# Performance work log

Hardware: AMD Instinct MI355X
Metric: run time of the kernel (lower is better)

Reference implementation:

```python
import jax, jax.numpy as jnp
import numpy as np

B, S, P, G, E = 16, 1024, 32, 64, 512
HD = E // 2          # head_dim = 256
SCALE = HD ** -0.5
LAMBDA_INIT = 0.8 - 0.6 * float(np.exp(-0.3 * 0.0))  # depth=0 -> 0.2
EPS = 1e-5


def setup_inputs() -> dict:
    key = jax.random.key(0)
    ks = jax.random.split(key, 12)
    inp = {
        'query': jax.random.normal(ks[0], (B, S, E), jnp.float32),
        'key': jax.random.normal(ks[1], (B, P, G, E), jnp.float32),
        'mask': jax.random.randint(ks[2], (B, S), 0, 2).astype(bool),
        'Wq': jax.random.normal(ks[3], (E, E), jnp.float32) * (E ** -0.5),
        'Wk': jax.random.normal(ks[4], (E, E), jnp.float32) * (E ** -0.5),
        'Wv': jax.random.normal(ks[5], (E, E), jnp.float32) * (E ** -0.5),
        'Wo': jax.random.normal(ks[6], (E, E), jnp.float32) * (E ** -0.5),
        'lq1': jax.random.normal(ks[7], (HD,), jnp.float32) * 0.1,
        'lk1': jax.random.normal(ks[8], (HD,), jnp.float32) * 0.1,
        'lq2': jax.random.normal(ks[9], (HD,), jnp.float32) * 0.1,
        'lk2': jax.random.normal(ks[10], (HD,), jnp.float32) * 0.1,
        'gamma': jnp.ones((E,), jnp.float32),
    }
    return inp


def reference(query, key, mask, Wq, Wk, Wv, Wo, lq1, lk1, lq2, lk2, gamma):
    b, s, e = query.shape
    _, p, g, _ = key.shape
    L = p * g
    key2d = key.reshape(b, L, e)

    Q = (query @ Wq).reshape(b, s, 2, HD).transpose(0, 2, 1, 3) * SCALE  # [B,2,S,hd]
    K = (key2d @ Wk).reshape(b, L, 2, HD).transpose(0, 2, 1, 3)          # [B,2,L,hd]
    V = key2d @ Wv                                                       # [B,L,E]

    scores = jnp.einsum('bhsd,bhld->bhsl', Q, K)                         # [B,2,S,L]
    # masked_fill(~mask, 0.0) with mask broadcast [B,1,S,1]
    scores = jnp.where(mask[:, None, :, None], scores, 0.0)
    attn = jax.nn.softmax(scores, axis=-1)

    lam1 = jnp.exp(jnp.sum(lq1 * lk1))
    lam2 = jnp.exp(jnp.sum(lq2 * lk2))
    lam = lam1 - lam2 + LAMBDA_INIT

    diff = attn[:, 0] - lam * attn[:, 1]                                 # [B,S,L]
    out2d = jnp.einsum('bsl,ble->bse', diff, V)                          # [B,S,E]

    # RMSNorm over last dim with affine gamma
    rms = out2d * jax.lax.rsqrt(jnp.mean(out2d * out2d, axis=-1, keepdims=True) + EPS)
    rms = rms * gamma
    out = (rms * (1.0 - LAMBDA_INIT)) @ Wo                               # [B,S,E]

    return out, diff.reshape(b, s, p, g)
```

## Files before the change

kernel.cpp:

```cpp
#include <hip/hip_runtime.h>
#include <hip/hip_bf16.h>


typedef short short8 __attribute__((ext_vector_type(8)));
typedef __bf16 bf16x8 __attribute__((ext_vector_type(8)));
typedef float f32x4 __attribute__((ext_vector_type(4)));

#define LDS_BYTES 16384
#define OUT0_ELEMS 8388608L

__global__ void probe_kernel(const void* gamma, const void* mask, int* flags)
{
    if (threadIdx.x == 0) {
        unsigned g = *(const unsigned*)gamma;
        flags[0] = (g == 0x3F800000u) ? 1 : 0;
        flags[1] = 0;
    }
    __syncthreads();
    const unsigned* mi = (const unsigned*)mask;
    int bad = 0;
    for (int i = threadIdx.x; i < 4096; i += blockDim.x)
        if (mi[i] > 1u) bad = 1;
    if (bad) atomicOr(&flags[1], 1);
}

__global__ void convert_mask(const void* __restrict__ mask, int* __restrict__ mi,
                             const int* __restrict__ flags)
{
    int i = blockIdx.x * 256 + threadIdx.x;
    if (flags[1]) mi[i] = ((const unsigned char*)mask)[i] ? 1 : 0;
    else          mi[i] = ((const int*)mask)[i] ? 1 : 0;
}

__device__ __forceinline__ float read_elem(const void* p, int i, int isf32)
{
    return isf32 ? ((const float*)p)[i]
                 : __bfloat162float(((const __hip_bfloat16*)p)[i]);
}

__global__ void convert_gamma(const void* __restrict__ gamma, float* __restrict__ g,
                              const int* __restrict__ flags)
{
    int i = blockIdx.x * 256 + threadIdx.x;
    g[i] = read_elem(gamma, i, flags[0]);
}

__global__ void transpose_w(const void* __restrict__ Wq, const void* __restrict__ Wk,
                            const void* __restrict__ Wv, const void* __restrict__ Wo,
                            __hip_bfloat16* __restrict__ dst, const int* __restrict__ flags)
{
    int which = blockIdx.y;
    const void* s = (which == 0) ? Wq : (which == 1) ? Wk : (which == 2) ? Wv : Wo;
    __hip_bfloat16* d = dst + (long)which * 262144;
    int idx = blockIdx.x * 256 + threadIdx.x;
    int k = idx >> 9, n = idx & 511;
    d[n * 512 + k] = __float2bfloat16(read_elem(s, idx, flags[0]));
}

__global__ void lam_kernel(const void* __restrict__ lq1, const void* __restrict__ lk1,
                           const void* __restrict__ lq2, const void* __restrict__ lk2,
                           float* __restrict__ lamp, const int* __restrict__ flags)
{
    int t = threadIdx.x;
    int f = flags[0];
    float s1 = 0.0f, s2 = 0.0f;
#pragma unroll
    for (int j = 0; j < 4; ++j) {
        int idx = t * 4 + j;
        s1 += read_elem(lq1, idx, f) * read_elem(lk1, idx, f);
        s2 += read_elem(lq2, idx, f) * read_elem(lk2, idx, f);
    }
#pragma unroll
    for (int off = 1; off < 64; off <<= 1) {
        s1 += __shfl_xor(s1, off);
        s2 += __shfl_xor(s2, off);
    }
    if (t == 0) *lamp = __expf(s1) - __expf(s2) + 0.2f;
}

__global__ void zero_lst(float* __restrict__ lst)
{
    lst[blockIdx.x * 256 + threadIdx.x] = 0.0f;
}

__device__ __forceinline__ void stage_u(const void* A, long aoff, int lda, int af32,
                                        const __hip_bfloat16* B, int ldb,
                                        int kt, char* smem, int tid)
{
    if (af32) {
#pragma unroll
        for (int j = 0; j < 2; ++j) {
            int chunk = j * 256 + tid;
            const float* g = (const float*)A + aoff + (long)(chunk >> 2) * lda + kt + (chunk & 3) * 8;
            f32x4 x0 = *(const f32x4*)g;
            f32x4 x1 = *(const f32x4*)(g + 4);
            __hip_bfloat16 tmp[8];
#pragma unroll
            for (int t = 0; t < 4; ++t) tmp[t] = __float2bfloat16(x0[t]);
#pragma unroll
            for (int t = 0; t < 4; ++t) tmp[4 + t] = __float2bfloat16(x1[t]);
            *(short8*)(smem + chunk * 16) = *(const short8*)tmp;
        }
    } else {
#pragma unroll
        for (int j = 0; j < 2; ++j) {
            int chunk = j * 256 + tid;
            const __hip_bfloat16* g = (const __hip_bfloat16*)A + aoff
                                    + (long)(chunk >> 2) * lda + kt + (chunk & 3) * 8;
            __builtin_amdgcn_global_load_lds(
                (__attribute__((address_space(1))) void*)g,
                (__attribute__((address_space(3))) void*)(smem + chunk * 16), 16, 0, 0);
        }
    }
#pragma unroll
    for (int j = 0; j < 2; ++j) {
        int chunk = j * 256 + tid;
        const __hip_bfloat16* g = B + (long)(chunk >> 2) * ldb + kt + (chunk & 3) * 8;
        __builtin_amdgcn_global_load_lds(
            (__attribute__((address_space(1))) void*)g,
            (__attribute__((address_space(3))) void*)(smem + 8192 + chunk * 16), 16, 0, 0);
    }
}

__device__ __forceinline__ void mfma_block(char* smem, int tid, f32x4 (&acc)[4][4])
{
    const int lane = tid & 63, wid = tid >> 6;
    const int wm = wid >> 1, wn = wid & 1;
    const int lm = lane & 15, lq = lane >> 4;
    short8 a[4], b[4];
#pragma unroll
    for (int i = 0; i < 4; ++i)
        a[i] = *(const short8*)(smem + (wm * 64 + i * 16 + lm) * 64 + lq * 16);
#pragma unroll
    for (int i = 0; i < 4; ++i)
        b[i] = *(const short8*)(smem + 8192 + (wn * 64 + i * 16 + lm) * 64 + lq * 16);
#pragma unroll
    for (int i = 0; i < 4; ++i)
#pragma unroll
        for (int j = 0; j < 4; ++j)
            acc[i][j] = __builtin_amdgcn_mfma_f32_16x16x32_bf16(
                __builtin_bit_cast(bf16x8, a[i]),
                __builtin_bit_cast(bf16x8, b[j]),
                acc[i][j], 0, 0, 0);
}

__device__ __forceinline__ void zero_acc(f32x4 (&acc)[4][4])
{
#pragma unroll
    for (int i = 0; i < 4; ++i)
#pragma unroll
        for (int j = 0; j < 4; ++j)
#pragma unroll
            for (int r = 0; r < 4; ++r) acc[i][j][r] = 0.0f;
}

__device__ __forceinline__ void tile_gemm_u(const void* A, long aoff, int lda, int af32,
                                            const __hip_bfloat16* B, int ldb, int K,
                                            char* smem, int tid, f32x4 (&acc)[4][4])
{
    zero_acc(acc);
    for (int kt = 0; kt < K; kt += 32) {
        __syncthreads();
        stage_u(A, aoff, lda, af32, B, ldb, kt, smem, tid);
        __syncthreads();
        mfma_block(smem, tid, acc);
    }
}

template <int MODE, int AF>
__launch_bounds__(256, 4)
__global__ void gemm_u(const void* __restrict__ A,
                       const __hip_bfloat16* __restrict__ B,
                       void* __restrict__ C,
                       int K, int lda, int ldb, int ldc,
                       long sA, long sB, long sC, float scale,
                       const int* __restrict__ flags)
{
    __shared__ __align__(16) char smem[LDS_BYTES];
    const int tid = threadIdx.x;
    const int bn = blockIdx.x, bm = blockIdx.y, bz = blockIdx.z;
    const int af32 = AF ? flags[0] : 0;
    const long aoff = (long)bz * sA + (long)bm * 128 * lda;
    const __hip_bfloat16* Bb = B + (long)bz * sB + (long)bn * 128 * ldb;

    f32x4 acc[4][4];
    tile_gemm_u(A, aoff, lda, af32, Bb, ldb, K, smem, tid, acc);

    const int f32o = (MODE == 3) ? flags[0] : 0;
    const int lane = tid & 63, wid = tid >> 6;
    const int wm = wid >> 1, wn = wid & 1;
    const int lm = lane & 15, lq = lane >> 4;
#pragma unroll
    for (int im = 0; im < 4; ++im)
#pragma unroll
        for (int in = 0; in < 4; ++in)
#pragma unroll
            for (int r = 0; r < 4; ++r) {
                int row = bm * 128 + wm * 64 + im * 16 + lq * 4 + r;
                int col = bn * 128 + wn * 64 + in * 16 + lm;
                float v = acc[im][in][r] * scale;
                if (MODE == 0) {
                    ((__hip_bfloat16*)C)[bz * sC + (long)row * ldc + col] = __float2bfloat16(v);
                } else if (MODE == 2) {
                    ((float*)C)[bz * sC + (long)row * ldc + col] = v;
                } else if (MODE == 3) {
                    long idx = bz * sC + (long)row * ldc + col;
                    if (f32o) ((float*)C)[idx] = v;
                    else      ((__hip_bfloat16*)C)[idx] = __float2bfloat16(v);
                } else {
                    int bb = row >> 11, l = row & 2047;
                    ((__hip_bfloat16*)C)[((long)bb * 512 + col) * 2048 + l] = __float2bfloat16(v);
                }
            }
}

__device__ __forceinline__ void score_epilogue(
    f32x4 (&acc)[4][4], char* smem, int tid,
    int nt, int st, int b, int bl, const int* __restrict__ mask,
    float* __restrict__ lstats, __hip_bfloat16* __restrict__ P, int h)
{
    const int lane = tid & 63, wid = tid >> 6;
    const int wm = wid >> 1, wn = wid & 1;
    const int lm = lane & 15, lq = lane >> 4;
    float esum[4][4];
#pragma unroll
    for (int im = 0; im < 4; ++im)
#pragma unroll
        for (int r = 0; r < 4; ++r) {
            int rl = wm * 64 + im * 16 + lq * 4 + r;
            int s  = st * 128 + rl;
            int mv = mask[b * 1024 + s];
            float es = 0.0f;
#pragma unroll
            for (int in = 0; in < 4; ++in) {
                int col = nt * 128 + wn * 64 + in * 16 + lm;
                float sc = mv ? acc[im][in][r] : 0.0f;
                float e  = __expf(sc);
                P[((long)bl * 1024 + s) * 2048 + col] = __float2bfloat16(e);
                float t = e;
                t += __shfl_xor(t, 1);
                t += __shfl_xor(t, 2);
                t += __shfl_xor(t, 4);
                t += __shfl_xor(t, 8);
                es += t;
            }
            esum[im][r] = es;
        }
    __syncthreads();
    float* red = (float*)smem;
    if (lm == 0) {
#pragma unroll
        for (int im = 0; im < 4; ++im)
#pragma unroll
            for (int r = 0; r < 4; ++r)
                red[wn * 128 + wm * 64 + im * 16 + lq * 4 + r] = esum[im][r];
    }
    __syncthreads();
    if (tid < 128)
        atomicAdd(&lstats[((long)(b * 2 + h)) * 1024 + st * 128 + tid],
                  red[tid] + red[128 + tid]);
}

__launch_bounds__(256, 3)
__global__ void score_kernel(const __hip_bfloat16* __restrict__ Q,
                             const __hip_bfloat16* __restrict__ Km,
                             const int* __restrict__ mask,
                             float* __restrict__ lstats,
                             __hip_bfloat16* __restrict__ P0,
                             __hip_bfloat16* __restrict__ P1,
                             int bbase)
{
    __shared__ __align__(16) char smem[LDS_BYTES];
    const int tid = threadIdx.x;
    const int nt = blockIdx.x, st = blockIdx.y, bl = blockIdx.z;
    const int b = bl + bbase;
    const long A0 = ((long)b * 1024 + st * 128) * 512;
    const __hip_bfloat16* B0 = Km + ((long)b * 2048 + nt * 128) * 512;

    f32x4 acc[4][4];
    tile_gemm_u(Q, A0, 512, 0, B0, 512, 256, smem, tid, acc);
    score_epilogue(acc, smem, tid, nt, st, b, bl, mask, lstats, P0, 0);
    tile_gemm_u(Q, A0 + 256, 512, 0, B0 + 256, 512, 256, smem, tid, acc);
    score_epilogue(acc, smem, tid, nt, st, b, bl, mask, lstats, P1, 1);
}

__global__ void finalize_kernel(__hip_bfloat16* P0,
                                const __hip_bfloat16* __restrict__ P1,
                                const float* __restrict__ lstats,
                                const float* __restrict__ lamp,
                                void* dout, int bbase,
                                const int* __restrict__ flags)
{
    const long row = blockIdx.x;
    const int bl = (int)(row >> 10), s = (int)(row & 1023);
    const int b  = bl + bbase;
    const int tid = threadIdx.x;
    const float lam = *lamp;
    const float i0 = 1.0f / lstats[((long)(b * 2)) * 1024 + s];
    const float i1 = lam  / lstats[((long)(b * 2 + 1)) * 1024 + s];
    const long lbase = row * 2048 + (long)tid * 8;

    union { short8 v; __hip_bfloat16 h[8]; } u0, u1, ub;
    u0.v = *(const short8*)(P0 + lbase);
    u1.v = *(const short8*)(P1 + lbase);
    float d[8];
#pragma unroll
    for (int j = 0; j < 8; ++j)
        d[j] = __bfloat162float(u0.h[j]) * i0 - __bfloat162float(u1.h[j]) * i1;

    const long gidx = ((long)b * 1024 + s) * 2048 + (long)tid * 8;
    if (flags[0]) {
        float* outF = (float*)dout + OUT0_ELEMS;
        f32x4 v0, v1;
#pragma unroll
        for (int j = 0; j < 4; ++j) { v0[j] = d[j]; v1[j] = d[4 + j]; }
        *(f32x4*)(outF + gidx)     = v0;
        *(f32x4*)(outF + gidx + 4) = v1;
    } else {
        __hip_bfloat16* outH = (__hip_bfloat16*)dout + OUT0_ELEMS;
        union { short8 v; __hip_bfloat16 h[8]; } uo;
#pragma unroll
        for (int j = 0; j < 8; ++j) uo.h[j] = __float2bfloat16(d[j]);
        *(short8*)(outH + gidx) = uo.v;
    }
#pragma unroll
    for (int j = 0; j < 8; ++j) ub.h[j] = __float2bfloat16(d[j]);
    *(short8*)(P0 + lbase) = ub.v;
}

__global__ void rmsnorm_kernel(const float* __restrict__ X,
                               const float* __restrict__ gamma,
                               __hip_bfloat16* __restrict__ Y)
{
    long row = blockIdx.x;
    int lane = threadIdx.x;
    const float* x = X + row * 512 + lane * 8;
    f32x4 v0 = *(const f32x4*)x;
    f32x4 v1 = *(const f32x4*)(x + 4);
    float ss = v0[0] * v0[0] + v0[1] * v0[1] + v0[2] * v0[2] + v0[3] * v0[3]
             + v1[0] * v1[0] + v1[1] * v1[1] + v1[2] * v1[2] + v1[3] * v1[3];
#pragma unroll
    for (int off = 1; off < 64; off <<= 1) ss += __shfl_xor(ss, off);
    float rinv = rsqrtf(ss * (1.0f / 512.0f) + 1e-5f) * 0.8f;
#pragma unroll
    for (int j = 0; j < 4; ++j)
        Y[row * 512 + lane * 8 + j] = __float2bfloat16(v0[j] * rinv * gamma[lane * 8 + j]);
#pragma unroll
    for (int j = 0; j < 4; ++j)
        Y[row * 512 + lane * 8 + 4 + j] = __float2bfloat16(v1[j] * rinv * gamma[lane * 8 + 4 + j]);
}

extern "C" void kernel_launch(void* const* d_in, const int* in_sizes, int n_in,
                              void* d_out, int out_size, void* d_ws, size_t ws_size,
                              hipStream_t stream)
{
    const void* query = d_in[0];
    const void* key2d = d_in[1];
    const void* maskp = d_in[2];
    const void* Wq    = d_in[3];
    const void* Wk    = d_in[4];
    const void* Wv    = d_in[5];
    const void* Wo    = d_in[6];
    const void* lq1   = d_in[7];
    const void* lk1   = d_in[8];
    const void* lq2   = d_in[9];
    const void* lk2   = d_in[10];
    const void* gamma = d_in[11];

    char* w = (char*)d_ws;
    __hip_bfloat16* WT    = (__hip_bfloat16*)(w);
    __hip_bfloat16* WqT   = WT;
    __hip_bfloat16* WkT   = WT + 262144;
    __hip_bfloat16* WvT   = WT + 524288;
    __hip_bfloat16* WoT   = WT + 786432;
    float*          lamp  = (float*)(w + 2097152);
    int*            flags = (int*)(w + 2097216);
    float*          gammaF= (float*)(w + 2097280);
    int*            maskI = (int*)(w + 2162688);
    __hip_bfloat16* Qb    = (__hip_bfloat16*)(w + 2228224);
    __hip_bfloat16* Kb    = (__hip_bfloat16*)(w + 19005440);
    __hip_bfloat16* Vt    = (__hip_bfloat16*)(w + 52559872);
    float*          lst   = (float*)(w + 86114304);
    float*          o2d   = (float*)(w + 86245376);
    __hip_bfloat16* rmsb  = (__hip_bfloat16*)(w + 119799808);
    __hip_bfloat16* diffBF= (__hip_bfloat16*)(w + 136577024);
    __hip_bfloat16* P1s   = (__hip_bfloat16*)(w + 103022592);

    const bool hugews = ws_size >= 270794752UL;
    const bool bigws  = ws_size >= 203685888UL;

    probe_kernel<<<1, 256, 0, stream>>>(gamma, maskp, flags);
    convert_mask<<<64, 256, 0, stream>>>(maskp, maskI, flags);
    convert_gamma<<<2, 256, 0, stream>>>(gamma, gammaF, flags);
    transpose_w<<<dim3(1024, 4, 1), 256, 0, stream>>>(Wq, Wk, Wv, Wo, WT, flags);
    lam_kernel<<<1, 64, 0, stream>>>(lq1, lk1, lq2, lk2, lamp, flags);
    zero_lst<<<128, 256, 0, stream>>>(lst);

    gemm_u<0, 1><<<dim3(4, 128, 1), 256, 0, stream>>>(query, WqT, Qb,
        512, 512, 512, 512, 0, 0, 0, 0.0625f, flags);
    gemm_u<0, 1><<<dim3(4, 256, 1), 256, 0, stream>>>(key2d, WkT, Kb,
        512, 512, 512, 512, 0, 0, 0, 1.0f, flags);
    gemm_u<1, 1><<<dim3(4, 256, 1), 256, 0, stream>>>(key2d, WvT, Vt,
        512, 512, 512, 0, 0, 0, 0, 1.0f, flags);

    if (hugews) {
        __hip_bfloat16* P0f = diffBF;
        __hip_bfloat16* P1f = diffBF + 33554432L;
        score_kernel<<<dim3(16, 8, 16), 256, 0, stream>>>(Qb, Kb, maskI, lst,
            P0f, P1f, 0);
        finalize_kernel<<<16384, 256, 0, stream>>>(P0f, P1f, lst, lamp,
            d_out, 0, flags);
        gemm_u<2, 0><<<dim3(4, 8, 16), 256, 0, stream>>>(P0f, Vt, o2d,
            2048, 2048, 2048, 512, 1024L * 2048, 512L * 2048, 1024L * 512, 1.0f, flags);
    } else if (bigws) {
        __hip_bfloat16* P0h = diffBF;
        __hip_bfloat16* P1h = diffBF + 16777216L;
        for (int h = 0; h < 2; ++h) {
            int bb = h * 8;
            score_kernel<<<dim3(16, 8, 8), 256, 0, stream>>>(Qb, Kb, maskI, lst,
                P0h, P1h, bb);
            finalize_kernel<<<8192, 256, 0, stream>>>(P0h, P1h, lst, lamp,
                d_out, bb, flags);
            gemm_u<2, 0><<<dim3(4, 8, 8), 256, 0, stream>>>(P0h,
                Vt + (long)bb * 512 * 2048, o2d + (long)bb * 1024 * 512,
                2048, 2048, 2048, 512, 1024L * 2048, 512L * 2048, 1024L * 512, 1.0f, flags);
        }
    } else {
        __hip_bfloat16* scratch = (__hip_bfloat16*)d_out;
        for (int h = 0; h < 2; ++h) {
            int bb = h * 8;
            score_kernel<<<dim3(16, 8, 8), 256, 0, stream>>>(Qb, Kb, maskI, lst,
                scratch, P1s, bb);
            finalize_kernel<<<8192, 256, 0, stream>>>(scratch, P1s, lst, lamp,
                d_out, bb, flags);
            gemm_u<2, 0><<<dim3(4, 8, 8), 256, 0, stream>>>(scratch,
                Vt + (long)bb * 512 * 2048, o2d + (long)bb * 1024 * 512,
                2048, 2048, 2048, 512, 1024L * 2048, 512L * 2048, 1024L * 512, 1.0f, flags);
        }
    }

    rmsnorm_kernel<<<16384, 64, 0, stream>>>(o2d, gammaF, rmsb);

    gemm_u<3, 0><<<dim3(4, 128, 1), 256, 0, stream>>>(rmsb, WoT, d_out,
        512, 512, 512, 512, 0, 0, 1024L * 512, 1.0f, flags);
}
```

Before: 632.7 us.

## Merge prep kernels into one launch and fuse K and V projection GEMMs

Five small setup kernels (mask conversion, gamma conversion, weight transpose, lambda, stats zeroing) are merged into a single block-dispatched prep kernel to cut launch overhead. The separate K and V projection GEMMs are replaced by one kv_gemm that stages the shared key tile once per k-step and computes both K and V accumulators. This halves the reads and fp32-to-bf16 conversion of the key input, at the cost of doubled accumulator registers and more LDS per block, which may lower occupancy.

```diff
diff --git a/kernel.cpp b/kernel.cpp
--- a/kernel.cpp
+++ b/kernel.cpp
@@ -24,63 +24,57 @@
     if (bad) atomicOr(&flags[1], 1);
 }
 
-__global__ void convert_mask(const void* __restrict__ mask, int* __restrict__ mi,
-                             const int* __restrict__ flags)
-{
-    int i = blockIdx.x * 256 + threadIdx.x;
-    if (flags[1]) mi[i] = ((const unsigned char*)mask)[i] ? 1 : 0;
-    else          mi[i] = ((const int*)mask)[i] ? 1 : 0;
-}
-
 __device__ __forceinline__ float read_elem(const void* p, int i, int isf32)
 {
     return isf32 ? ((const float*)p)[i]
                  : __bfloat162float(((const __hip_bfloat16*)p)[i]);
 }
 
-__global__ void convert_gamma(const void* __restrict__ gamma, float* __restrict__ g,
-                              const int* __restrict__ flags)
-{
-    int i = blockIdx.x * 256 + threadIdx.x;
-    g[i] = read_elem(gamma, i, flags[0]);
-}
-
-__global__ void transpose_w(const void* __restrict__ Wq, const void* __restrict__ Wk,
+__global__ void prep_kernel(const void* __restrict__ mask, int* __restrict__ maskI,
+                            const void* __restrict__ gamma, float* __restrict__ gammaF,
+                            const void* __restrict__ Wq, const void* __restrict__ Wk,
                             const void* __restrict__ Wv, const void* __restrict__ Wo,
-                            __hip_bfloat16* __restrict__ dst, const int* __restrict__ flags)
-{
-    int which = blockIdx.y;
-    const void* s = (which == 0) ? Wq : (which == 1) ? Wk : (which == 2) ? Wv : Wo;
-    __hip_bfloat16* d = dst + (long)which * 262144;
-    int idx = blockIdx.x * 256 + threadIdx.x;
-    int k = idx >> 9, n = idx & 511;
-    d[n * 512 + k] = __float2bfloat16(read_elem(s, idx, flags[0]));
-}
-
-__global__ void lam_kernel(const void* __restrict__ lq1, const void* __restrict__ lk1,
-                           const void* __restrict__ lq2, const void* __restrict__ lk2,
-                           float* __restrict__ lamp, const int* __restrict__ flags)
-{
-    int t = threadIdx.x;
-    int f = flags[0];
-    float s1 = 0.0f, s2 = 0.0f;
-#pragma unroll
-    for (int j = 0; j < 4; ++j) {
-        int idx = t * 4 + j;
-        s1 += read_elem(lq1, idx, f) * read_elem(lk1, idx, f);
-        s2 += read_elem(lq2, idx, f) * read_elem(lk2, idx, f);
-    }
-#pragma unroll
-    for (int off = 1; off < 64; off <<= 1) {
-        s1 += __shfl_xor(s1, off);
-        s2 += __shfl_xor(s2, off);
-    }
-    if (t == 0) *lamp = __expf(s1) - __expf(s2) + 0.2f;
-}
-
-__global__ void zero_lst(float* __restrict__ lst)
-{
-    lst[blockIdx.x * 256 + threadIdx.x] = 0.0f;
+                            __hip_bfloat16* __restrict__ WT,
+                            const void* __restrict__ lq1, const void* __restrict__ lk1,
+                            const void* __restrict__ lq2, const void* __restrict__ lk2,
+                            float* __restrict__ lamp, float* __restrict__ lst,
+                            const int* __restrict__ flags)
+{
+    const int bid = blockIdx.x, tid = threadIdx.x;
+    const int f = flags[0];
+    if (bid < 4096) {
+        int which = bid >> 10;
+        const void* s = (which == 0) ? Wq : (which == 1) ? Wk : (which == 2) ? Wv : Wo;
+        __hip_bfloat16* d = WT + (long)which * 262144;
+        int idx = (bid & 1023) * 256 + tid;
+        int k = idx >> 9, n = idx & 511;
+        d[n * 512 + k] = __float2bfloat16(read_elem(s, idx, f));
+    } else if (bid < 4160) {
+        int i = (bid - 4096) * 256 + tid;
+        if (flags[1]) maskI[i] = ((const unsigned char*)mask)[i] ? 1 : 0;
+        else          maskI[i] = ((const int*)mask)[i] ? 1 : 0;
+    } else if (bid < 4162) {
+        int i = (bid - 4160) * 256 + tid;
+        gammaF[i] = read_elem(gamma, i, f);
+    } else if (bid < 4290) {
+        lst[(bid - 4162) * 256 + tid] = 0.0f;
+    } else {
+        if (tid < 64) {
+            float s1 = 0.0f, s2 = 0.0f;
+#pragma unroll
+            for (int j = 0; j < 4; ++j) {
+                int idx = tid * 4 + j;
+                s1 += read_elem(lq1, idx, f) * read_elem(lk1, idx, f);
+                s2 += read_elem(lq2, idx, f) * read_elem(lk2, idx, f);
+            }
+#pragma unroll
+            for (int off = 1; off < 64; off <<= 1) {
+                s1 += __shfl_xor(s1, off);
+                s2 += __shfl_xor(s2, off);
+            }
+            if (tid == 0) *lamp = __expf(s1) - __expf(s2) + 0.2f;
+        }
+    }
 }
 
 __device__ __forceinline__ void stage_u(const void* A, long aoff, int lda, int af32,
@@ -211,6 +205,112 @@
                     int bb = row >> 11, l = row & 2047;
                     ((__hip_bfloat16*)C)[((long)bb * 512 + col) * 2048 + l] = __float2bfloat16(v);
                 }
+            }
+}
+
+__launch_bounds__(256, 2)
+__global__ void kv_gemm(const void* __restrict__ A,
+                        const __hip_bfloat16* __restrict__ Bk,
+                        const __hip_bfloat16* __restrict__ Bv,
+                        __hip_bfloat16* __restrict__ Kb,
+                        __hip_bfloat16* __restrict__ Vt,
+                        const int* __restrict__ flags)
+{
+    __shared__ __align__(16) char smem[24576];
+    const int tid = threadIdx.x;
+    const int bn = blockIdx.x, bm = blockIdx.y;
+    const int af32 = flags[0];
+    const long aoff = (long)bm * 128 * 512;
+    const __hip_bfloat16* Bkb = Bk + (long)bn * 128 * 512;
+    const __hip_bfloat16* Bvb = Bv + (long)bn * 128 * 512;
+
+    f32x4 acck[4][4], accv[4][4];
+    zero_acc(acck); zero_acc(accv);
+
+    const int lane = tid & 63, wid = tid >> 6;
+    const int wm = wid >> 1, wn = wid & 1;
+    const int lm = lane & 15, lq = lane >> 4;
+
+    for (int kt = 0; kt < 512; kt += 32) {
+        __syncthreads();
+        if (af32) {
+#pragma unroll
+            for (int j = 0; j < 2; ++j) {
+                int chunk = j * 256 + tid;
+                const float* g = (const float*)A + aoff + (long)(chunk >> 2) * 512 + kt + (chunk & 3) * 8;
+                f32x4 x0 = *(const f32x4*)g;
+                f32x4 x1 = *(const f32x4*)(g + 4);
+                __hip_bfloat16 tmp[8];
+#pragma unroll
+                for (int t = 0; t < 4; ++t) tmp[t] = __float2bfloat16(x0[t]);
+#pragma unroll
+                for (int t = 0; t < 4; ++t) tmp[4 + t] = __float2bfloat16(x1[t]);
+                *(short8*)(smem + chunk * 16) = *(const short8*)tmp;
+            }
+        } else {
+#pragma unroll
+            for (int j = 0; j < 2; ++j) {
+                int chunk = j * 256 + tid;
+                const __hip_bfloat16* g = (const __hip_bfloat16*)A + aoff
+                                        + (long)(chunk >> 2) * 512 + kt + (chunk & 3) * 8;
+                __builtin_amdgcn_global_load_lds(
+                    (__attribute__((address_space(1))) void*)g,
+                    (__attribute__((address_space(3))) void*)(smem + chunk * 16), 16, 0, 0);
+            }
+        }
+#pragma unroll
+        for (int j = 0; j < 2; ++j) {
+            int chunk = j * 256 + tid;
+            const __hip_bfloat16* gk = Bkb + (long)(chunk >> 2) * 512 + kt + (chunk & 3) * 8;
+            __builtin_amdgcn_global_load_lds(
+                (__attribute__((address_space(1))) void*)gk,
+                (__attribute__((address_space(3))) void*)(smem + 8192 + chunk * 16), 16, 0, 0);
+        }
+#pragma unroll
+        for (int j = 0; j < 2; ++j) {
+            int chunk = j * 256 + tid;
+            const __hip_bfloat16* gv = Bvb + (long)(chunk >> 2) * 512 + kt + (chunk & 3) * 8;
+            __builtin_amdgcn_global_load_lds(
+                (__attribute__((address_space(1))) void*)gv,
+                (__attribute__((address_space(3))) void*)(smem + 16384 + chunk * 16), 16, 0, 0);
+        }
+        __syncthreads();
+        short8 a[4], bk[4], bv[4];
+#pragma unroll
+        for (int i = 0; i < 4; ++i)
+            a[i] = *(const short8*)(smem + (wm * 64 + i * 16 + lm) * 64 + lq * 16);
+#pragma unroll
+        for (int i = 0; i < 4; ++i)
+            bk[i] = *(const short8*)(smem + 8192 + (wn * 64 + i * 16 + lm) * 64 + lq * 16);
+#pragma unroll
+        for (int i = 0; i < 4; ++i)
+            bv[i] = *(const short8*)(smem + 16384 + (wn * 64 + i * 16 + lm) * 64 + lq * 16);
+#pragma unroll
+        for (int i = 0; i < 4; ++i)
+#pragma unroll
+            for (int j = 0; j < 4; ++j) {
+                acck[i][j] = __builtin_amdgcn_mfma_f32_16x16x32_bf16(
+                    __builtin_bit_cast(bf16x8, a[i]),
+                    __builtin_bit_cast(bf16x8, bk[j]),
+                    acck[i][j], 0, 0, 0);
+                accv[i][j] = __builtin_amdgcn_mfma_f32_16x16x32_bf16(
+                    __builtin_bit_cast(bf16x8, a[i]),
+                    __builtin_bit_cast(bf16x8, bv[j]),
+                    accv[i][j], 0, 0, 0);
+            }
+    }
+
+#pragma unroll
+    for (int im = 0; im < 4; ++im)
+#pragma unroll
+        for (int in = 0; in < 4; ++in)
+#pragma unroll
+            for (int r = 0; r < 4; ++r) {
+                int row = bm * 128 + wm * 64 + im * 16 + lq * 4 + r;
+                int col = bn * 128 + wn * 64 + in * 16 + lm;
+                Kb[(long)row * 512 + col] = __float2bfloat16(acck[im][in][r]);
+                int bb = row >> 11, l = row & 2047;
+                Vt[((long)bb * 512 + col) * 2048 + l] = __float2bfloat16(accv[im][in][r]);
             }
 }
 
@@ -390,18 +490,12 @@
     const bool bigws  = ws_size >= 203685888UL;
 
     probe_kernel<<<1, 256, 0, stream>>>(gamma, maskp, flags);
-    convert_mask<<<64, 256, 0, stream>>>(maskp, maskI, flags);
-    convert_gamma<<<2, 256, 0, stream>>>(gamma, gammaF, flags);
-    transpose_w<<<dim3(1024, 4, 1), 256, 0, stream>>>(Wq, Wk, Wv, Wo, WT, flags);
-    lam_kernel<<<1, 64, 0, stream>>>(lq1, lk1, lq2, lk2, lamp, flags);
-    zero_lst<<<128, 256, 0, stream>>>(lst);
+    prep_kernel<<<4291, 256, 0, stream>>>(maskp, maskI, gamma, gammaF,
+        Wq, Wk, Wv, Wo, WT, lq1, lk1, lq2, lk2, lamp, lst, flags);
 
     gemm_u<0, 1><<<dim3(4, 128, 1), 256, 0, stream>>>(query, WqT, Qb,
         512, 512, 512, 512, 0, 0, 0, 0.0625f, flags);
-    gemm_u<0, 1><<<dim3(4, 256, 1), 256, 0, stream>>>(key2d, WkT, Kb,
-        512, 512, 512, 512, 0, 0, 0, 1.0f, flags);
-    gemm_u<1, 1><<<dim3(4, 256, 1), 256, 0, stream>>>(key2d, WvT, Vt,
-        512, 512, 512, 0, 0, 0, 0, 1.0f, flags);
+    kv_gemm<<<dim3(4, 256), 256, 0, stream>>>(key2d, WkT, WvT, Kb, Vt, flags);
 
     if (hugews) {
         __hip_bfloat16* P0f = diffBF;
```

Result: no change. 629.0 us (-0.6%).
